# Optimization experiments

Hardware: AMD Instinct MI355X
Metric: run time of the kernel (lower is better)

## Reference

```python
import jax, jax.numpy as jnp
import numpy as np


def gcn_conv(x, src, dst, ew, W, b):
    """PyG GCNConv with edge weights: add self-loops, symmetric deg norm,
    x @ W then normalized scatter-add aggregation, plus bias."""
    N = x.shape[0]
    loop = jnp.arange(N)
    src2 = jnp.concatenate([src, loop])
    dst2 = jnp.concatenate([dst, loop])
    ew2 = jnp.concatenate([ew, jnp.ones((N,), dtype=x.dtype)])
    deg = jax.ops.segment_sum(ew2, dst2, num_segments=N)
    dis = jnp.where(deg > 0, jax.lax.rsqrt(jnp.maximum(deg, 1e-30)), 0.0)
    norm = dis[src2] * ew2 * dis[dst2]            # [E+N]
    h = x @ W                                      # [N, F]
    msg = h[src2] * norm[:, None]                  # gather + scale
    out = jax.ops.segment_sum(msg, dst2, num_segments=N)  # scatter-add
    return out + b


def setup_inputs() -> dict:
    key = jax.random.key(0)
    ks = jax.random.split(key, 12)
    N, F, E, H = 50000, 128, 625000, 121
    x = jax.random.normal(ks[0], (N, F), dtype=jnp.float32)
    edge_index = jax.random.randint(ks[1], (2, E), 0, N, dtype=jnp.int64)
    edge_attr = jax.random.uniform(ks[2], (E,), dtype=jnp.float32)
    s = 1.0 / np.sqrt(F)
    W1 = jax.random.uniform(ks[3], (F, F), minval=-s, maxval=s)
    b1 = jnp.zeros((F,), dtype=jnp.float32)
    W2 = jax.random.uniform(ks[4], (F, F), minval=-s, maxval=s)
    b2 = jnp.zeros((F,), dtype=jnp.float32)
    lw1 = jax.random.uniform(ks[5], (F, H), minval=-s, maxval=s)
    lb1 = jax.random.uniform(ks[6], (H,), minval=-s, maxval=s)
    sh = 1.0 / np.sqrt(H)
    lw2 = jax.random.uniform(ks[7], (H, 1), minval=-sh, maxval=sh)
    lb2 = jax.random.uniform(ks[8], (1,), minval=-sh, maxval=sh)
    return {"x": x, "edge_index": edge_index, "edge_attr": edge_attr,
            "W1": W1, "b1": b1, "W2": W2, "b2": b2,
            "lw1": lw1, "lb1": lb1, "lw2": lw2, "lb2": lb2}


def reference(x, edge_index, edge_attr, W1, b1, W2, b2, lw1, lb1, lw2, lb2):
    src, dst = edge_index[0], edge_index[1]
    h = jax.nn.relu(gcn_conv(x, src, dst, edge_attr, W1, b1))
    h = jax.nn.relu(gcn_conv(h, src, dst, edge_attr, W2, b2))
    g = jnp.mean(h, axis=0)                        # graph readout [F]
    g = jax.nn.relu(g @ lw1 + lb1)
    return g @ lw2 + lb2                           # [1]
```

## Files before the change

kernel.cpp:

```cpp
#include <hip/hip_runtime.h>
#include <hip/hip_bf16.h>

#define FDIM 128
#define ELLW 64

typedef unsigned int uint;
typedef unsigned short ushort;
typedef unsigned char uchar;
typedef __attribute__((ext_vector_type(8))) short bf16x8;
typedef __attribute__((ext_vector_type(4))) float f32x4;

__device__ __forceinline__ ushort f2bf(float f) {
    uint u = __float_as_uint(f);
    return (ushort)((u + 0x7fffu + ((u >> 16) & 1u)) >> 16);
}
__device__ __forceinline__ float bfhi(uint v) { return __uint_as_float(v & 0xffff0000u); }
__device__ __forceinline__ uchar f2fp8(float f) {
    return (uchar)(__builtin_amdgcn_cvt_pk_fp8_f32(f, 0.f, 0, false) & 0xff);
}

__global__ void prep(const float* __restrict__ W1, const float* __restrict__ W2,
                     ushort* __restrict__ wt1, ushort* __restrict__ wt2,
                     int* __restrict__ cnt, int N) {
    int i = blockIdx.x * 256 + threadIdx.x;
    if (i < 16384) {
        int k = i >> 7, c = i & 127;
        wt1[c * FDIM + k] = f2bf(W1[i]);
    } else {
        int j = i - 16384;
        int k = j >> 7, c = j & 127;
        wt2[c * FDIM + k] = f2bf(W2[j]);
    }
    for (int j = i; j < N; j += 32768) cnt[j] = 0;
}

__global__ void hist_fill(const int* __restrict__ srcs,
                          const int* __restrict__ dsts,
                          const float* __restrict__ ew,
                          int* cnt, uint* __restrict__ ell, int E) {
    int e = blockIdx.x * blockDim.x + threadIdx.x;
    if (e >= E) return;
    int d = dsts[e];
    int r = atomicAdd(&cnt[d], 1);
    if (r < ELLW)
        ell[(long)d * ELLW + r] = ((uint)f2bf(ew[e]) << 16) | (uint)srcs[e];
}

__global__ void deg_dis(const int* __restrict__ cnt,
                        const uint* __restrict__ ell,
                        float* __restrict__ dis, int N) {
    int i = blockIdx.x * blockDim.x + threadIdx.x;
    if (i >= N) return;
    int c = min(cnt[i], ELLW);
    const uint* row = ell + (long)i * ELLW;
    float s = 1.0f;
    for (int k = 0; k < c; ++k) s += bfhi(row[k]);
    dis[i] = rsqrtf(s);
}

template<int IN_BF16>
__global__ __launch_bounds__(256) void gemm_mfma(const void* __restrict__ Ap,
                                                 const ushort* __restrict__ Wt,
                                                 const float* __restrict__ dis,
                                                 uchar* __restrict__ Hb, int N) {
    int lane = threadIdx.x & 63;
    int wave = threadIdx.x >> 6;
    int row0 = blockIdx.x * 64 + wave * 16;
    int m = lane & 15;
    int ko = (lane >> 4) << 3;
    int row = row0 + m;

    f32x4 acc[8];
    #pragma unroll
    for (int n = 0; n < 8; ++n) acc[n] = (f32x4){0.f, 0.f, 0.f, 0.f};

    #pragma unroll 1
    for (int kc = 0; kc < FDIM; kc += 32) {
        bf16x8 a = (bf16x8)(short)0;
        if (row < N) {
            if (IN_BF16) {
                a = *(const bf16x8*)((const ushort*)Ap + (long)row * FDIM + kc + ko);
            } else {
                const float* A = (const float*)Ap;
                float4 f0 = *(const float4*)(A + (long)row * FDIM + kc + ko);
                float4 f1 = *(const float4*)(A + (long)row * FDIM + kc + ko + 4);
                a[0] = (short)f2bf(f0.x); a[1] = (short)f2bf(f0.y);
                a[2] = (short)f2bf(f0.z); a[3] = (short)f2bf(f0.w);
                a[4] = (short)f2bf(f1.x); a[5] = (short)f2bf(f1.y);
                a[6] = (short)f2bf(f1.z); a[7] = (short)f2bf(f1.w);
            }
        }
        #pragma unroll
        for (int n = 0; n < 8; ++n) {
            bf16x8 b = *(const bf16x8*)(Wt + (n * 16 + m) * FDIM + kc + ko);
            acc[n] = __builtin_amdgcn_mfma_f32_16x16x32_bf16(a, b, acc[n], 0, 0, 0);
        }
    }

    int rbase = (lane >> 4) << 2;
    #pragma unroll
    for (int r = 0; r < 4; ++r) {
        int gr = row0 + rbase + r;
        if (gr < N) {
            float sc = dis[gr];
            #pragma unroll
            for (int n = 0; n < 8; ++n)
                Hb[(long)gr * FDIM + n * 16 + m] = f2fp8(acc[n][r] * sc);
        }
    }
}

template<int FUSE>
__global__ __launch_bounds__(256)
void aggregate(const uchar* __restrict__ hb,
               const float* __restrict__ dis,
               const float* __restrict__ b,
               const int* __restrict__ cnt,
               const uint* __restrict__ ell,
               ushort* __restrict__ Ob,
               float* __restrict__ partial, int N) {
    __shared__ float4 red[8][32];
    int tid = threadIdx.x;
    int lane = tid & 31;
    int grp = tid >> 5;
    int d = blockIdx.x * 8 + grp;
    float4 rsum = make_float4(0.f, 0.f, 0.f, 0.f);

    if (d < N) {
        float dd = dis[d];
        float4 bv = ((const float4*)b)[lane];
        const uint* row = ell + (long)d * ELLW;
        int end = min(cnt[d], ELLW);
        float4 acc = make_float4(0.f, 0.f, 0.f, 0.f);
        int k = 0;
        for (; k + 3 < end; k += 4) {
            uint e0 = row[k],     e1 = row[k + 1];
            uint e2 = row[k + 2], e3 = row[k + 3];
            int s0 = e0 & 0xffff, s1 = e1 & 0xffff;
            int s2 = e2 & 0xffff, s3 = e3 & 0xffff;
            float w0 = bfhi(e0), w1 = bfhi(e1);
            float w2 = bfhi(e2), w3 = bfhi(e3);
            uint u0 = *(const uint*)(hb + (long)s0 * FDIM + lane * 4);
            uint u1 = *(const uint*)(hb + (long)s1 * FDIM + lane * 4);
            uint u2 = *(const uint*)(hb + (long)s2 * FDIM + lane * 4);
            uint u3 = *(const uint*)(hb + (long)s3 * FDIM + lane * 4);
            {   auto lo = __builtin_amdgcn_cvt_pk_f32_fp8(u0, false);
                auto hi = __builtin_amdgcn_cvt_pk_f32_fp8(u0, true);
                acc.x = fmaf(lo[0], w0, acc.x); acc.y = fmaf(lo[1], w0, acc.y);
                acc.z = fmaf(hi[0], w0, acc.z); acc.w = fmaf(hi[1], w0, acc.w); }
            {   auto lo = __builtin_amdgcn_cvt_pk_f32_fp8(u1, false);
                auto hi = __builtin_amdgcn_cvt_pk_f32_fp8(u1, true);
                acc.x = fmaf(lo[0], w1, acc.x); acc.y = fmaf(lo[1], w1, acc.y);
                acc.z = fmaf(hi[0], w1, acc.z); acc.w = fmaf(hi[1], w1, acc.w); }
            {   auto lo = __builtin_amdgcn_cvt_pk_f32_fp8(u2, false);
                auto hi = __builtin_amdgcn_cvt_pk_f32_fp8(u2, true);
                acc.x = fmaf(lo[0], w2, acc.x); acc.y = fmaf(lo[1], w2, acc.y);
                acc.z = fmaf(hi[0], w2, acc.z); acc.w = fmaf(hi[1], w2, acc.w); }
            {   auto lo = __builtin_amdgcn_cvt_pk_f32_fp8(u3, false);
                auto hi = __builtin_amdgcn_cvt_pk_f32_fp8(u3, true);
                acc.x = fmaf(lo[0], w3, acc.x); acc.y = fmaf(lo[1], w3, acc.y);
                acc.z = fmaf(hi[0], w3, acc.z); acc.w = fmaf(hi[1], w3, acc.w); }
        }
        for (; k < end; ++k) {
            uint e0 = row[k];
            int s0 = e0 & 0xffff;
            float w0 = bfhi(e0);
            uint u0 = *(const uint*)(hb + (long)s0 * FDIM + lane * 4);
            auto lo = __builtin_amdgcn_cvt_pk_f32_fp8(u0, false);
            auto hi = __builtin_amdgcn_cvt_pk_f32_fp8(u0, true);
            acc.x = fmaf(lo[0], w0, acc.x); acc.y = fmaf(lo[1], w0, acc.y);
            acc.z = fmaf(hi[0], w0, acc.z); acc.w = fmaf(hi[1], w0, acc.w);
        }
        uint ud = *(const uint*)(hb + (long)d * FDIM + lane * 4);
        auto slo = __builtin_amdgcn_cvt_pk_f32_fp8(ud, false);
        auto shi = __builtin_amdgcn_cvt_pk_f32_fp8(ud, true);
        float4 o;
        o.x = fmaf(slo[0] + acc.x, dd, bv.x);
        o.y = fmaf(slo[1] + acc.y, dd, bv.y);
        o.z = fmaf(shi[0] + acc.z, dd, bv.z);
        o.w = fmaf(shi[1] + acc.w, dd, bv.w);
        o.x = fmaxf(o.x, 0.f); o.y = fmaxf(o.y, 0.f);
        o.z = fmaxf(o.z, 0.f); o.w = fmaxf(o.w, 0.f);
        if (FUSE) {
            rsum = o;
        } else {
            uint2 ov;
            ov.x = (uint)f2bf(o.x) | ((uint)f2bf(o.y) << 16);
            ov.y = (uint)f2bf(o.z) | ((uint)f2bf(o.w) << 16);
            *(uint2*)(Ob + (long)d * FDIM + lane * 4) = ov;
        }
    }

    if (FUSE) {
        red[grp][lane] = rsum;
        __syncthreads();
        if (tid < FDIM) {
            float s = 0.f;
            #pragma unroll
            for (int g = 0; g < 8; ++g)
                s += ((const float*)&red[g][tid >> 2])[tid & 3];
            partial[(long)blockIdx.x * FDIM + tid] = s;
        }
    }
}

__global__ void reduce_g(const float* __restrict__ partial,
                         float* __restrict__ partial2, int nb) {
    __shared__ float sd[2][FDIM];
    int col = threadIdx.x & 127;
    int half = threadIdx.x >> 7;
    float s = 0.f;
    for (int r = blockIdx.x * 2 + half; r < nb; r += 128)
        s += partial[(long)r * FDIM + col];
    sd[half][col] = s;
    __syncthreads();
    if (threadIdx.x < FDIM)
        partial2[(long)blockIdx.x * FDIM + col] = sd[0][col] + sd[1][col];
}

__global__ void mlp_head(const float* __restrict__ partial2,
                         const float* __restrict__ lw1,
                         const float* __restrict__ lb1,
                         const float* __restrict__ lw2,
                         const float* __restrict__ lb2,
                         float* __restrict__ out, float invN, int H) {
    __shared__ float gs[FDIM];
    __shared__ float red[FDIM];
    int t = threadIdx.x;
    float s = 0.f;
    #pragma unroll 8
    for (int r = 0; r < 64; ++r) s += partial2[r * FDIM + t];
    gs[t] = s * invN;
    __syncthreads();
    float p = 0.f;
    if (t < H) {
        float acc = lb1[t];
        #pragma unroll 8
        for (int f = 0; f < FDIM; ++f)
            acc = fmaf(gs[f], lw1[f * H + t], acc);
        p = fmaxf(acc, 0.f) * lw2[t];
    }
    red[t] = p;
    __syncthreads();
    for (int st = 64; st > 0; st >>= 1) {
        if (t < st) red[t] += red[t + st];
        __syncthreads();
    }
    if (t == 0) out[0] = red[0] + lb2[0];
}

extern "C" void kernel_launch(void* const* d_in, const int* in_sizes, int n_in,
                              void* d_out, int out_size, void* d_ws, size_t ws_size,
                              hipStream_t stream) {
    const float* x   = (const float*)d_in[0];
    const int*   eix = (const int*)d_in[1];
    const float* ea  = (const float*)d_in[2];
    const float* W1  = (const float*)d_in[3];
    const float* b1  = (const float*)d_in[4];
    const float* W2  = (const float*)d_in[5];
    const float* b2  = (const float*)d_in[6];
    const float* lw1 = (const float*)d_in[7];
    const float* lb1 = (const float*)d_in[8];
    const float* lw2 = (const float*)d_in[9];
    const float* lb2 = (const float*)d_in[10];

    const int N = in_sizes[0] / FDIM;
    const int E = in_sizes[2];
    const int H = in_sizes[8];
    const int* srcs = eix;
    const int* dsts = eix + E;

    int nAgg = (N + 7) / 8;

    uchar*  hb      = (uchar*)d_ws;
    ushort* ob      = (ushort*)(hb + (long)N * FDIM);
    ushort* wt1     = ob + (long)N * FDIM;
    ushort* wt2     = wt1 + FDIM * FDIM;
    float*  partial = (float*)(wt2 + FDIM * FDIM);
    float*  partial2= partial + (long)nAgg * FDIM;
    float*  dis     = partial2 + 64 * FDIM;
    uint*   ell     = (uint*)(dis + N);
    int*    cnt     = (int*)(ell + (long)N * ELLW);

    float* outv = (float*)d_out;

    int nb = (N + 255) / 256;
    int eb = (E + 255) / 256;
    int gemmBlocks = (N + 63) / 64;

    prep<<<128, 256, 0, stream>>>(W1, W2, wt1, wt2, cnt, N);
    hist_fill<<<eb, 256, 0, stream>>>(srcs, dsts, ea, cnt, ell, E);
    deg_dis<<<nb, 256, 0, stream>>>(cnt, ell, dis, N);

    gemm_mfma<0><<<gemmBlocks, 256, 0, stream>>>(x, wt1, dis, hb, N);
    aggregate<0><<<nAgg, 256, 0, stream>>>(hb, dis, b1, cnt, ell, ob, partial, N);

    gemm_mfma<1><<<gemmBlocks, 256, 0, stream>>>(ob, wt2, dis, hb, N);
    aggregate<1><<<nAgg, 256, 0, stream>>>(hb, dis, b2, cnt, ell, ob, partial, N);

    reduce_g<<<64, 256, 0, stream>>>(partial, partial2, nAgg);
    mlp_head<<<1, FDIM, 0, stream>>>(partial2, lw1, lb1, lw2, lb2, outv,
                                     1.0f / (float)N, H);
}
```

Before: 162.1 us.

## Widen aggregation gathers to 16-byte loads with 8 lanes per node

The aggregate kernel now assigns 8 threads per destination node, each handling 16 features, instead of 32 threads with 4 features each. It also reads ELL rows and fp8 feature rows with 16-byte vector loads, so fewer, wider memory instructions are issued per gathered neighbor. The deg_dis kernel likewise reads ELL entries as uint4. The trade-offs are more registers per thread, less parallelism spread across each row, and a larger shared reduction buffer with a 32-way column sum.

```diff
diff --git a/kernel.cpp b/kernel.cpp
--- a/kernel.cpp
+++ b/kernel.cpp
@@ -52,9 +52,15 @@
     int i = blockIdx.x * blockDim.x + threadIdx.x;
     if (i >= N) return;
     int c = min(cnt[i], ELLW);
+    const uint4* row4 = (const uint4*)(ell + (long)i * ELLW);
+    float s = 1.0f;
+    int k4 = 0;
+    for (; k4 * 4 + 3 < c; ++k4) {
+        uint4 u = row4[k4];
+        s += bfhi(u.x) + bfhi(u.y) + bfhi(u.z) + bfhi(u.w);
+    }
     const uint* row = ell + (long)i * ELLW;
-    float s = 1.0f;
-    for (int k = 0; k < c; ++k) s += bfhi(row[k]);
+    for (int k = k4 * 4; k < c; ++k) s += bfhi(row[k]);
     dis[i] = rsqrtf(s);
 }
 
@@ -110,6 +116,27 @@
     }
 }
 
+__device__ __forceinline__ void cvt4_acc(uint4 u, float wv,
+                                         float4& a0, float4& a1,
+                                         float4& a2, float4& a3) {
+    auto lo0 = __builtin_amdgcn_cvt_pk_f32_fp8(u.x, false);
+    auto hi0 = __builtin_amdgcn_cvt_pk_f32_fp8(u.x, true);
+    auto lo1 = __builtin_amdgcn_cvt_pk_f32_fp8(u.y, false);
+    auto hi1 = __builtin_amdgcn_cvt_pk_f32_fp8(u.y, true);
+    auto lo2 = __builtin_amdgcn_cvt_pk_f32_fp8(u.z, false);
+    auto hi2 = __builtin_amdgcn_cvt_pk_f32_fp8(u.z, true);
+    auto lo3 = __builtin_amdgcn_cvt_pk_f32_fp8(u.w, false);
+    auto hi3 = __builtin_amdgcn_cvt_pk_f32_fp8(u.w, true);
+    a0.x = fmaf(lo0[0], wv, a0.x); a0.y = fmaf(lo0[1], wv, a0.y);
+    a0.z = fmaf(hi0[0], wv, a0.z); a0.w = fmaf(hi0[1], wv, a0.w);
+    a1.x = fmaf(lo1[0], wv, a1.x); a1.y = fmaf(lo1[1], wv, a1.y);
+    a1.z = fmaf(hi1[0], wv, a1.z); a1.w = fmaf(hi1[1], wv, a1.w);
+    a2.x = fmaf(lo2[0], wv, a2.x); a2.y = fmaf(lo2[1], wv, a2.y);
+    a2.z = fmaf(hi2[0], wv, a2.z); a2.w = fmaf(hi2[1], wv, a2.w);
+    a3.x = fmaf(lo3[0], wv, a3.x); a3.y = fmaf(lo3[1], wv, a3.y);
+    a3.z = fmaf(hi3[0], wv, a3.z); a3.w = fmaf(hi3[1], wv, a3.w);
+}
+
 template<int FUSE>
 __global__ __launch_bounds__(256)
 void aggregate(const uchar* __restrict__ hb,
@@ -119,86 +146,94 @@
                const uint* __restrict__ ell,
                ushort* __restrict__ Ob,
                float* __restrict__ partial, int N) {
-    __shared__ float4 red[8][32];
+    __shared__ float red[32][FDIM];
     int tid = threadIdx.x;
-    int lane = tid & 31;
-    int grp = tid >> 5;
-    int d = blockIdx.x * 8 + grp;
-    float4 rsum = make_float4(0.f, 0.f, 0.f, 0.f);
+    int lane = tid & 7;
+    int grp = tid >> 3;
+    int d = blockIdx.x * 32 + grp;
+    int c0 = lane * 16;
+    float4 o0, o1, o2, o3;
 
     if (d < N) {
         float dd = dis[d];
-        float4 bv = ((const float4*)b)[lane];
-        const uint* row = ell + (long)d * ELLW;
+        float4 bv0 = ((const float4*)b)[lane * 4];
+        float4 bv1 = ((const float4*)b)[lane * 4 + 1];
+        float4 bv2 = ((const float4*)b)[lane * 4 + 2];
+        float4 bv3 = ((const float4*)b)[lane * 4 + 3];
+        const uint4* row4 = (const uint4*)(ell + (long)d * ELLW);
         int end = min(cnt[d], ELLW);
-        float4 acc = make_float4(0.f, 0.f, 0.f, 0.f);
+        float4 a0 = make_float4(0.f, 0.f, 0.f, 0.f);
+        float4 a1 = a0, a2 = a0, a3 = a0;
         int k = 0;
         for (; k + 3 < end; k += 4) {
-            uint e0 = row[k],     e1 = row[k + 1];
-            uint e2 = row[k + 2], e3 = row[k + 3];
-            int s0 = e0 & 0xffff, s1 = e1 & 0xffff;
-            int s2 = e2 & 0xffff, s3 = e3 & 0xffff;
-            float w0 = bfhi(e0), w1 = bfhi(e1);
-            float w2 = bfhi(e2), w3 = bfhi(e3);
-            uint u0 = *(const uint*)(hb + (long)s0 * FDIM + lane * 4);
-            uint u1 = *(const uint*)(hb + (long)s1 * FDIM + lane * 4);
-            uint u2 = *(const uint*)(hb + (long)s2 * FDIM + lane * 4);
-            uint u3 = *(const uint*)(hb + (long)s3 * FDIM + lane * 4);
-            {   auto lo = __builtin_amdgcn_cvt_pk_f32_fp8(u0, false);
-                auto hi = __builtin_amdgcn_cvt_pk_f32_fp8(u0, true);
-                acc.x = fmaf(lo[0], w0, acc.x); acc.y = fmaf(lo[1], w0, acc.y);
-                acc.z = fmaf(hi[0], w0, acc.z); acc.w = fmaf(hi[1], w0, acc.w); }
-            {   auto lo = __builtin_amdgcn_cvt_pk_f32_fp8(u1, false);
-                auto hi = __builtin_amdgcn_cvt_pk_f32_fp8(u1, true);
-                acc.x = fmaf(lo[0], w1, acc.x); acc.y = fmaf(lo[1], w1, acc.y);
-                acc.z = fmaf(hi[0], w1, acc.z); acc.w = fmaf(hi[1], w1, acc.w); }
-            {   auto lo = __builtin_amdgcn_cvt_pk_f32_fp8(u2, false);
-                auto hi = __builtin_amdgcn_cvt_pk_f32_fp8(u2, true);
-                acc.x = fmaf(lo[0], w2, acc.x); acc.y = fmaf(lo[1], w2, acc.y);
-                acc.z = fmaf(hi[0], w2, acc.z); acc.w = fmaf(hi[1], w2, acc.w); }
-            {   auto lo = __builtin_amdgcn_cvt_pk_f32_fp8(u3, false);
-                auto hi = __builtin_amdgcn_cvt_pk_f32_fp8(u3, true);
-                acc.x = fmaf(lo[0], w3, acc.x); acc.y = fmaf(lo[1], w3, acc.y);
-                acc.z = fmaf(hi[0], w3, acc.z); acc.w = fmaf(hi[1], w3, acc.w); }
-        }
+            uint4 ev = row4[k >> 2];
+            int s0 = ev.x & 0xffff, s1 = ev.y & 0xffff;
+            int s2 = ev.z & 0xffff, s3 = ev.w & 0xffff;
+            float w0 = bfhi(ev.x), w1 = bfhi(ev.y);
+            float w2 = bfhi(ev.z), w3 = bfhi(ev.w);
+            uint4 u0 = *(const uint4*)(hb + (long)s0 * FDIM + c0);
+            uint4 u1 = *(const uint4*)(hb + (long)s1 * FDIM + c0);
+            uint4 u2 = *(const uint4*)(hb + (long)s2 * FDIM + c0);
+            uint4 u3 = *(const uint4*)(hb + (long)s3 * FDIM + c0);
+            cvt4_acc(u0, w0, a0, a1, a2, a3);
+            cvt4_acc(u1, w1, a0, a1, a2, a3);
+            cvt4_acc(u2, w2, a0, a1, a2, a3);
+            cvt4_acc(u3, w3, a0, a1, a2, a3);
+        }
+        const uint* row = ell + (long)d * ELLW;
         for (; k < end; ++k) {
             uint e0 = row[k];
             int s0 = e0 & 0xffff;
             float w0 = bfhi(e0);
-            uint u0 = *(const uint*)(hb + (long)s0 * FDIM + lane * 4);
-            auto lo = __builtin_amdgcn_cvt_pk_f32_fp8(u0, false);
-            auto hi = __builtin_amdgcn_cvt_pk_f32_fp8(u0, true);
-            acc.x = fmaf(lo[0], w0, acc.x); acc.y = fmaf(lo[1], w0, acc.y);
-            acc.z = fmaf(hi[0], w0, acc.z); acc.w = fmaf(hi[1], w0, acc.w);
-        }
-        uint ud = *(const uint*)(hb + (long)d * FDIM + lane * 4);
-        auto slo = __builtin_amdgcn_cvt_pk_f32_fp8(ud, false);
-        auto shi = __builtin_amdgcn_cvt_pk_f32_fp8(ud, true);
-        float4 o;
-        o.x = fmaf(slo[0] + acc.x, dd, bv.x);
-        o.y = fmaf(slo[1] + acc.y, dd, bv.y);
-        o.z = fmaf(shi[0] + acc.z, dd, bv.z);
-        o.w = fmaf(shi[1] + acc.w, dd, bv.w);
-        o.x = fmaxf(o.x, 0.f); o.y = fmaxf(o.y, 0.f);
-        o.z = fmaxf(o.z, 0.f); o.w = fmaxf(o.w, 0.f);
-        if (FUSE) {
-            rsum = o;
-        } else {
-            uint2 ov;
-            ov.x = (uint)f2bf(o.x) | ((uint)f2bf(o.y) << 16);
-            ov.y = (uint)f2bf(o.z) | ((uint)f2bf(o.w) << 16);
-            *(uint2*)(Ob + (long)d * FDIM + lane * 4) = ov;
-        }
+            uint4 u0 = *(const uint4*)(hb + (long)s0 * FDIM + c0);
+            cvt4_acc(u0, w0, a0, a1, a2, a3);
+        }
+        uint4 ud = *(const uint4*)(hb + (long)d * FDIM + c0);
+        cvt4_acc(ud, 1.0f, a0, a1, a2, a3);
+        o0.x = fmaxf(fmaf(a0.x, dd, bv0.x), 0.f);
+        o0.y = fmaxf(fmaf(a0.y, dd, bv0.y), 0.f);
+        o0.z = fmaxf(fmaf(a0.z, dd, bv0.z), 0.f);
+        o0.w = fmaxf(fmaf(a0.w, dd, bv0.w), 0.f);
+        o1.x = fmaxf(fmaf(a1.x, dd, bv1.x), 0.f);
+        o1.y = fmaxf(fmaf(a1.y, dd, bv1.y), 0.f);
+        o1.z = fmaxf(fmaf(a1.z, dd, bv1.z), 0.f);
+        o1.w = fmaxf(fmaf(a1.w, dd, bv1.w), 0.f);
+        o2.x = fmaxf(fmaf(a2.x, dd, bv2.x), 0.f);
+        o2.y = fmaxf(fmaf(a2.y, dd, bv2.y), 0.f);
+        o2.z = fmaxf(fmaf(a2.z, dd, bv2.z), 0.f);
+        o2.w = fmaxf(fmaf(a2.w, dd, bv2.w), 0.f);
+        o3.x = fmaxf(fmaf(a3.x, dd, bv3.x), 0.f);
+        o3.y = fmaxf(fmaf(a3.y, dd, bv3.y), 0.f);
+        o3.z = fmaxf(fmaf(a3.z, dd, bv3.z), 0.f);
+        o3.w = fmaxf(fmaf(a3.w, dd, bv3.w), 0.f);
+        if (!FUSE) {
+            uint4 ov;
+            ov.x = (uint)f2bf(o0.x) | ((uint)f2bf(o0.y) << 16);
+            ov.y = (uint)f2bf(o0.z) | ((uint)f2bf(o0.w) << 16);
+            ov.z = (uint)f2bf(o1.x) | ((uint)f2bf(o1.y) << 16);
+            ov.w = (uint)f2bf(o1.z) | ((uint)f2bf(o1.w) << 16);
+            *(uint4*)(Ob + (long)d * FDIM + c0) = ov;
+            ov.x = (uint)f2bf(o2.x) | ((uint)f2bf(o2.y) << 16);
+            ov.y = (uint)f2bf(o2.z) | ((uint)f2bf(o2.w) << 16);
+            ov.z = (uint)f2bf(o3.x) | ((uint)f2bf(o3.y) << 16);
+            ov.w = (uint)f2bf(o3.z) | ((uint)f2bf(o3.w) << 16);
+            *(uint4*)(Ob + (long)d * FDIM + c0 + 8) = ov;
+        }
+    } else {
+        o0 = make_float4(0.f, 0.f, 0.f, 0.f);
+        o1 = o0; o2 = o0; o3 = o0;
     }
 
     if (FUSE) {
-        red[grp][lane] = rsum;
+        *(float4*)&red[grp][c0]      = o0;
+        *(float4*)&red[grp][c0 + 4]  = o1;
+        *(float4*)&red[grp][c0 + 8]  = o2;
+        *(float4*)&red[grp][c0 + 12] = o3;
         __syncthreads();
         if (tid < FDIM) {
             float s = 0.f;
             #pragma unroll
-            for (int g = 0; g < 8; ++g)
-                s += ((const float*)&red[g][tid >> 2])[tid & 3];
+            for (int g = 0; g < 32; ++g) s += red[g][tid];
             partial[(long)blockIdx.x * FDIM + tid] = s;
         }
     }
@@ -270,7 +305,7 @@
     const int* srcs = eix;
     const int* dsts = eix + E;
 
-    int nAgg = (N + 7) / 8;
+    int nAgg = (N + 31) / 32;
 
     uchar*  hb      = (uchar*)d_ws;
     ushort* ob      = (ushort*)(hb + (long)N * FDIM);
```

After: 144.6 us. 10.8% less time.
